# Optimization experiments

Hardware: AMD Instinct MI355X
Metric: run time of the kernel (lower is better)

## Reference

```python
import jax, jax.numpy as jnp
import numpy as np

HID = 2048      # hidden_size
NH = 16         # num_attention_heads
QLR = 1536      # q_lora_rank
KVLR = 512      # kv_lora_rank
DN = 128        # qk_nope_head_dim
DR = 64         # qk_rope_head_dim
DQK = DN + DR   # qk_head_dim = 192
DV = 128        # v_head_dim
EPS = 1e-6
THETA = 10000.0
B, T = 2, 2048


def rmsnorm(x, scale):
    return x * jax.lax.rsqrt(jnp.mean(x * x, axis=-1, keepdims=True) + EPS) * scale


def rope(x, positions):
    # x: [B, T, h, d]; NeoX-style rotate-half RoPE on the rope slice only
    d = x.shape[-1]
    inv_freq = 1.0 / (THETA ** (jnp.arange(0, d, 2, dtype=jnp.float32) / d))
    ang = positions.astype(jnp.float32)[..., None] * inv_freq       # [B, T, d/2]
    cos = jnp.cos(ang)[:, :, None, :]
    sin = jnp.sin(ang)[:, :, None, :]
    x1, x2 = jnp.split(x, 2, axis=-1)
    return jnp.concatenate([x1 * cos - x2 * sin, x2 * cos + x1 * sin], axis=-1).astype(x.dtype)


def setup_inputs() -> dict:
    key = jax.random.key(0)
    ks = jax.random.split(key, 8)
    s = 0.02
    x = jax.random.normal(ks[0], (B, T, HID), dtype=jnp.float32)
    attention_mask = jnp.ones((B, T), dtype=bool)
    positions = jnp.broadcast_to(jnp.arange(T, dtype=jnp.int32), (B, T))
    wqa = jax.random.normal(ks[1], (HID, QLR), dtype=jnp.float32) * s
    qa_scale = jnp.ones((QLR,), dtype=jnp.float32)
    wqb = jax.random.normal(ks[2], (QLR, NH * DQK), dtype=jnp.float32) * s
    wkva = jax.random.normal(ks[3], (HID, KVLR + DR), dtype=jnp.float32) * s
    kva_scale = jnp.ones((KVLR,), dtype=jnp.float32)
    wkvb = jax.random.normal(ks[4], (KVLR, NH * (DN + DV)), dtype=jnp.float32) * s
    wo = jax.random.normal(ks[5], (NH * DV, HID), dtype=jnp.float32) * s
    return {"x": x, "attention_mask": attention_mask, "positions": positions,
            "wqa": wqa, "qa_scale": qa_scale, "wqb": wqb,
            "wkva": wkva, "kva_scale": kva_scale, "wkvb": wkvb, "wo": wo}


def reference(x, attention_mask, positions, wqa, qa_scale, wqb, wkva, kva_scale, wkvb, wo):
    Bv, Tv, _ = x.shape
    # low-rank Q: hid -> q_lora_rank -> rmsnorm -> heads*qk_head_dim
    q = (rmsnorm(x @ wqa, qa_scale) @ wqb).reshape(Bv, Tv, NH, DQK)
    q_pass, q_rot = q[..., :DN], q[..., DN:]
    # compressed KV + shared rope key
    ckv = x @ wkva                                    # [B, T, KVLR + DR]
    kv_lat, k_rot = ckv[..., :KVLR], ckv[..., KVLR:].reshape(Bv, Tv, 1, DR)
    kv = (rmsnorm(kv_lat, kva_scale) @ wkvb).reshape(Bv, Tv, NH, DN + DV)
    k_pass, v = kv[..., :DN], kv[..., DN:]
    # decoupled RoPE on rope slice only
    q_rot = rope(q_rot, positions)
    k_rot = jnp.broadcast_to(rope(k_rot, positions), (Bv, Tv, NH, DR))
    q = jnp.concatenate([q_pass, q_rot], axis=-1)     # [B, T, H, 192]
    k = jnp.concatenate([k_pass, k_rot], axis=-1)
    # masked causal SDPA; v padding in the original is a no-op mathematically
    scale = DQK ** -0.5
    scores = jnp.einsum('bqhd,bkhd->bhqk', q, k) * scale
    causal = jnp.tril(jnp.ones((Tv, Tv), dtype=bool))
    mask = causal[None, None, :, :] & attention_mask[:, None, None, :].astype(bool)
    scores = jnp.where(mask, scores, jnp.finfo(scores.dtype).min)
    probs = jax.nn.softmax(scores, axis=-1)
    out = jnp.einsum('bhqk,bkhd->bqhd', probs, v).reshape(Bv, Tv, NH * DV)
    return out @ wo
```

## Files before the change

### kernel.cpp

```cpp
#include <hip/hip_runtime.h>
#include <math.h>
#include <stdint.h>

#define NHEAD 16
#define HIDDIM 2048
#define QLRANK 1536
#define KVRANK 512
#define DROT 64
#define BB 2
#define TT 2048
#define BTOK (BB*TT)
#define NPROJ 2304
#define CKV0 1536
#define ROT0 2048

typedef __bf16 bf16x8 __attribute__((ext_vector_type(8)));
typedef __bf16 bf16x4 __attribute__((ext_vector_type(4)));
typedef float f32x4 __attribute__((ext_vector_type(4)));
typedef uint16_t u16;
typedef uint32_t u32;

__device__ __forceinline__ u16 f2bf(float f) {
  union { float f; uint32_t u; } v; v.f = f;
  uint32_t r = v.u + 0x7fffu + ((v.u >> 16) & 1u);
  return (u16)(r >> 16);
}
__device__ __forceinline__ float bf2f(u16 h) {
  union { uint32_t u; float f; } v; v.u = ((uint32_t)h) << 16;
  return v.f;
}

__device__ __forceinline__ void gload_lds16(const u16* g, u16* l) {
  __builtin_amdgcn_global_load_lds(
      (const __attribute__((address_space(1))) uint32_t*)g,
      (__attribute__((address_space(3))) uint32_t*)l, 16, 0, 0);
}

__global__ __launch_bounds__(256) void cvt_f32_bf16(const float* __restrict__ in,
                                                    u16* __restrict__ out, int n) {
  int idx = (blockIdx.x * 256 + threadIdx.x) * 8;
  if (idx >= n) return;
  f32x4 a = *(const f32x4*)&in[idx];
  f32x4 b = *(const f32x4*)&in[idx + 4];
  union { f32x4 q; u16 e[8]; } w;
#pragma unroll
  for (int j = 0; j < 4; ++j) { w.e[j] = f2bf(a[j]); w.e[4 + j] = f2bf(b[j]); }
  *(f32x4*)&out[idx] = w.q;
}

__global__ __launch_bounds__(256) void transpose_w(const float* __restrict__ W,
                                                   u16* __restrict__ Wt,
                                                   int K, int N, int Npad, float scale,
                                                   const float* __restrict__ svec) {
  __shared__ float tile[32][33];
  int k0 = blockIdx.x * 32, n0 = blockIdx.y * 32;
  int tx = threadIdx.x, ty = threadIdx.y;
#pragma unroll
  for (int r = 0; r < 32; r += 8) {
    int k = k0 + ty + r, n = n0 + tx;
    tile[ty + r][tx] = (k < K && n < N) ? W[(size_t)k * N + n] : 0.f;
  }
  __syncthreads();
  float sv = scale * (svec ? svec[k0 + tx] : 1.f);
#pragma unroll
  for (int r = 0; r < 32; r += 8) {
    int n = n0 + ty + r, k = k0 + tx;
    if (n < Npad && k < K) Wt[(size_t)n * K + k] = f2bf(tile[tx][ty + r] * sv);
  }
}

template<int D>
__global__ __launch_bounds__(256) void row_invrms(const u16* __restrict__ in, int stride,
                                                  float* __restrict__ out) {
  const int row = blockIdx.x;
  const int tid = threadIdx.x;
  constexpr int NC = D / 8;
  float ss = 0.f;
  if (tid < NC) {
    union { f32x4 q; u16 e[8]; } t;
    t.q = *(const f32x4*)&in[(size_t)row * stride + tid * 8];
#pragma unroll
    for (int j = 0; j < 8; ++j) { float v = bf2f(t.e[j]); ss += v * v; }
  }
#pragma unroll
  for (int off = 1; off < 64; off <<= 1) ss += __shfl_xor(ss, off);
  __shared__ float red[4];
  if ((tid & 63) == 0) red[tid >> 6] = ss;
  __syncthreads();
  if (tid == 0)
    out[row] = rsqrtf((red[0] + red[1] + red[2] + red[3]) / (float)D + 1e-6f);
}

template<int OUTF32>
__global__ __launch_bounds__(256) void gemm_bt(const u16* __restrict__ A, int lda,
                                               const u16* __restrict__ Bt,
                                               void* __restrict__ Cv, int ldc,
                                               const float* __restrict__ rowscale,
                                               int N, int K) {
  __shared__ __align__(16) u16 As[2][128 * 32];
  __shared__ __align__(16) u16 Bs[2][128 * 32];
  const int tid = threadIdx.x;
  const int lane = tid & 63;
  const int wave = tid >> 6;
  const int bm = blockIdx.y * 128;
  const int bn = blockIdx.x * 128;
  const int wr = wave >> 1;
  const int wc = wave & 1;

  f32x4 acc[4][4] = {};

  const int srow = wave * 16 + (lane >> 2);
  const int scol = (lane & 3) * 8;
  const u16* Ag = A + (size_t)(bm + srow) * lda + scol;
  const u16* Bg = Bt + (size_t)(bn + srow) * K + scol;
  const int soff = (wave * 16) * 32;

  const int a_off = (wr * 64 + (lane & 15)) * 32 + (lane >> 4) * 8;
  const int b_off = (wc * 64 + (lane & 15)) * 32 + (lane >> 4) * 8;

  const int nt = K >> 5;

  gload_lds16(Ag, &As[0][soff]);
  gload_lds16(Ag + (size_t)64 * lda, &As[0][soff + 64 * 32]);
  gload_lds16(Bg, &Bs[0][soff]);
  gload_lds16(Bg + (size_t)64 * K, &Bs[0][soff + 64 * 32]);
  __syncthreads();

  int cur = 0;
  for (int t = 0; t < nt; ++t) {
    if (t + 1 < nt) {
      const int k0 = (t + 1) << 5;
      gload_lds16(Ag + k0, &As[cur ^ 1][soff]);
      gload_lds16(Ag + (size_t)64 * lda + k0, &As[cur ^ 1][soff + 64 * 32]);
      gload_lds16(Bg + k0, &Bs[cur ^ 1][soff]);
      gload_lds16(Bg + (size_t)64 * K + k0, &Bs[cur ^ 1][soff + 64 * 32]);
    }
    bf16x8 af[4], bfr[4];
#pragma unroll
    for (int m = 0; m < 4; ++m) af[m] = *(const bf16x8*)&As[cur][a_off + m * 16 * 32];
#pragma unroll
    for (int n = 0; n < 4; ++n) bfr[n] = *(const bf16x8*)&Bs[cur][b_off + n * 16 * 32];
#pragma unroll
    for (int m = 0; m < 4; ++m)
#pragma unroll
      for (int n = 0; n < 4; ++n)
        acc[m][n] = __builtin_amdgcn_mfma_f32_16x16x32_bf16(af[m], bfr[n], acc[m][n], 0, 0, 0);
    if (t + 1 < nt) {
      __syncthreads();
      cur ^= 1;
    }
  }

  const int row0 = bm + wr * 64 + (lane >> 4) * 4;
  const int col0 = bn + wc * 64 + (lane & 15);
#pragma unroll
  for (int m = 0; m < 4; ++m) {
    float rs[4] = {1.f, 1.f, 1.f, 1.f};
    if (rowscale) {
#pragma unroll
      for (int i = 0; i < 4; ++i) rs[i] = rowscale[row0 + m * 16 + i];
    }
#pragma unroll
    for (int n = 0; n < 4; ++n)
#pragma unroll
      for (int i = 0; i < 4; ++i) {
        size_t idx = (size_t)(row0 + m * 16 + i) * ldc + (col0 + n * 16);
        float v = acc[m][n][i] * rs[i];
        if (OUTF32) ((float*)Cv)[idx] = v;
        else        ((u16*)Cv)[idx] = f2bf(v);
      }
  }
}

template<int OUTF32>
__global__ __launch_bounds__(512, 2) void gemm256(const u16* __restrict__ A, int lda,
                                                  const u16* __restrict__ Bt,
                                                  void* __restrict__ Cv, int ldc,
                                                  const float* __restrict__ rowscale,
                                                  int K) {
  __shared__ __align__(16) u16 S[2][2][16384];
  const int tid = threadIdx.x, lane = tid & 63, wave = tid >> 6;
  const int l15 = lane & 15, l4 = lane >> 4;
  const int bm = blockIdx.y * 256, bn = blockIdx.x * 256;
  const int wm = wave >> 2, wn = wave & 3;

  const int rlo = lane >> 3;
  const int cbase = ((lane & 7) * 8) ^ ((lane >> 5) << 4);
  const u16* src[8];
  u16* dst[8];
#pragma unroll
  for (int j = 0; j < 8; ++j) {
    int gj = wave * 8 + j;
    if (gj < 32) {
      src[j] = A + (size_t)(bm + gj * 8 + rlo) * lda + cbase;
      dst[j] = &S[0][0][0] + gj * 512;
    } else {
      src[j] = Bt + (size_t)(bn + (gj - 32) * 8 + rlo) * K + cbase;
      dst[j] = &S[0][1][0] + (gj - 32) * 512;
    }
  }

  const int flip = ((l15 >> 2) & 1) << 5;
  const char* Sa0 = (const char*)&S[0][0][0] + wm * 16384;
  const char* Sb0 = (const char*)&S[0][1][0] + (wn >> 1) * 16384;
  const int arow0 = l15 * 128 + l4 * 16;
  const int brow0 = ((wn & 1) * 64 + l15) * 128 + l4 * 16;

  f32x4 acc[8][4] = {};
  const int nt = K >> 6;

#pragma unroll
  for (int j = 0; j < 8; ++j) gload_lds16(src[j], dst[j]);
#pragma unroll
  for (int j = 0; j < 8; ++j) gload_lds16(src[j] + 64, dst[j] + 32768);
  asm volatile("s_waitcnt vmcnt(8)" ::: "memory");
  __builtin_amdgcn_s_barrier();
  __builtin_amdgcn_sched_barrier(0);

  for (int t = 0; t < nt; ++t) {
    const char* Sab = Sa0 + (t & 1) * 65536;
    const char* Sbb = Sb0 + (t & 1) * 65536;
    bf16x8 bfr[4][2];
#pragma unroll
    for (int fn = 0; fn < 4; ++fn) {
      bfr[fn][0] = *(const bf16x8*)(Sbb + ((brow0 + fn * 2048) ^ flip));
      bfr[fn][1] = *(const bf16x8*)(Sbb + ((brow0 + fn * 2048 + 64) ^ flip));
    }
#pragma unroll
    for (int q = 0; q < 4; ++q) {
      bf16x8 a0[2], a1[2];
#pragma unroll
      for (int m2 = 0; m2 < 2; ++m2) {
        const int fm = q * 2 + m2;
        a0[m2] = *(const bf16x8*)(Sab + ((arow0 + fm * 2048) ^ flip));
        a1[m2] = *(const bf16x8*)(Sab + ((arow0 + fm * 2048 + 64) ^ flip));
      }
      __builtin_amdgcn_s_setprio(1);
#pragma unroll
      for (int m2 = 0; m2 < 2; ++m2)
#pragma unroll
        for (int fn = 0; fn < 4; ++fn) {
          f32x4 c = acc[q * 2 + m2][fn];
          c = __builtin_amdgcn_mfma_f32_16x16x32_bf16(a0[m2], bfr[fn][0], c, 0, 0, 0);
          c = __builtin_amdgcn_mfma_f32_16x16x32_bf16(a1[m2], bfr[fn][1], c, 0, 0, 0);
          acc[q * 2 + m2][fn] = c;
        }
      __builtin_amdgcn_s_setprio(0);
    }
    if (t + 1 < nt) {
      __builtin_amdgcn_s_barrier();
      __builtin_amdgcn_sched_barrier(0);
      if (t + 2 < nt) {
        const int koff = (t + 2) * 64;
#pragma unroll
        for (int j = 0; j < 8; ++j) gload_lds16(src[j] + koff, dst[j] + (t & 1) * 32768);
        asm volatile("s_waitcnt vmcnt(8)" ::: "memory");
      } else {
        asm volatile("s_waitcnt vmcnt(0)" ::: "memory");
      }
      __builtin_amdgcn_s_barrier();
      __builtin_amdgcn_sched_barrier(0);
    }
  }

  const int row0 = bm + wm * 128 + l4 * 4;
  const int col0 = bn + wn * 64 + l15;
#pragma unroll
  for (int fm = 0; fm < 8; ++fm) {
    float rs[4] = {1.f, 1.f, 1.f, 1.f};
    if (rowscale) {
#pragma unroll
      for (int i = 0; i < 4; ++i) rs[i] = rowscale[row0 + fm * 16 + i];
    }
#pragma unroll
    for (int fn = 0; fn < 4; ++fn)
#pragma unroll
      for (int i = 0; i < 4; ++i) {
        size_t idx = (size_t)(row0 + fm * 16 + i) * ldc + (col0 + fn * 16);
        float v = acc[fm][fn][i] * rs[i];
        if (OUTF32) ((float*)Cv)[idx] = v;
        else        ((u16*)Cv)[idx] = f2bf(v);
      }
  }
}

__global__ __launch_bounds__(256) void rope_table(const int* __restrict__ positions,
                                                  float2* __restrict__ tab) {
  int idx = blockIdx.x * 256 + threadIdx.x;
  if (idx >= BTOK * 32) return;
  int bt = idx >> 5, i = idx & 31;
  float invf = powf(10000.0f, -(float)i / 32.0f);
  float ang = (float)positions[bt] * invf;
  tab[idx] = make_float2(cosf(ang), sinf(ang));
}

__global__ __launch_bounds__(256) void rope_q(u16* __restrict__ q,
                                              const float2* __restrict__ tab) {
  int idx = blockIdx.x * 256 + threadIdx.x;
  if (idx >= BTOK * NHEAD * 32) return;
  int i = idx & 31;
  int h = (idx >> 5) & 15;
  int bt = idx >> 9;
  u16* p = q + (size_t)bt * 3072 + h * 192 + 128;
  float x1 = bf2f(p[i]), x2 = bf2f(p[32 + i]);
  float2 cs = tab[bt * 32 + i];
  p[i] = f2bf(x1 * cs.x - x2 * cs.y);
  p[32 + i] = f2bf(x2 * cs.x + x1 * cs.y);
}

__global__ __launch_bounds__(256) void assemble_k(const u16* __restrict__ kv,
                                                  const u16* __restrict__ proj,
                                                  const float2* __restrict__ tab,
                                                  u16* __restrict__ kf) {
  int bt = blockIdx.x;
  __shared__ __align__(16) u16 krot[64];
  int t = threadIdx.x;
  if (t < 64) {
    int i = t & 31;
    float2 cs = tab[bt * 32 + i];
    float x1 = bf2f(proj[(size_t)bt * NPROJ + ROT0 + i]);
    float x2 = bf2f(proj[(size_t)bt * NPROJ + ROT0 + 32 + i]);
    krot[t] = f2bf((t < 32) ? (x1 * cs.x - x2 * cs.y) : (x2 * cs.x + x1 * cs.y));
  }
  __syncthreads();
  for (int c = t; c < 16 * 24; c += 256) {
    int h = c / 24, seg = c % 24;
    u16* dst = kf + (size_t)bt * 3072 + h * 192 + seg * 8;
    if (seg < 16)
      *(f32x4*)dst = *(const f32x4*)&kv[(size_t)bt * 4096 + h * 256 + seg * 8];
    else
      *(f32x4*)dst = *(const f32x4*)&krot[(seg - 16) * 8];
  }
}

__device__ const int8_t JOB_QT[24] = {15,15,7,14,14,13,13,6,12,12,11,11,5,10,10,9,9,4,8,8,3,2,1,0};
__device__ const int8_t JOB_PC[24] = { 0, 1,2, 0, 1, 0, 1,2, 0, 1, 0, 1,2, 0, 1,0,1,2,0,1,2,2,2,2};

__global__ __launch_bounds__(256, 2) void attn_fwd5(const u16* __restrict__ Q,
                                                    const u16* __restrict__ Kf,
                                                    const u16* __restrict__ KV,
                                                    u16* __restrict__ O,
                                                    u16* __restrict__ Opart,
                                                    float2* __restrict__ ml) {
  __shared__ __align__(16) u16 Ks[2][64 * 192];
  __shared__ __align__(16) u16 Vs[2][64 * 128];

  const int tid = threadIdx.x, lane = tid & 63, wave = tid >> 6;
  const int l15 = lane & 15, l4 = lane >> 4;
  const int jobrank = blockIdx.x >> 5;
  const int bh = blockIdx.x & 31;
  const int qt = JOB_QT[jobrank];
  const int piece = JOB_PC[jobrank];
  const int q0 = qt * 128;
  const int b = bh >> 4, h = bh & 15;
  const int wq0 = q0 + wave * 32;

  bf16x8 qf[2][6];
#pragma unroll
  for (int m = 0; m < 2; ++m) {
    const u16* qp = Q + (size_t)(b * TT + wq0 + m * 16 + l15) * 3072 + h * 192 + l4 * 8;
#pragma unroll
    for (int kk = 0; kk < 6; ++kk) qf[m][kk] = *(const bf16x8*)(qp + kk * 32);
  }

  int ksrc[6];
#pragma unroll
  for (int j = 0; j < 6; ++j) {
    int o = (wave * 6 + j) * 1024 + lane * 16;
    int row = o / 384, col = o % 384;
    int scol = col ^ ((row & 7) << 4);
    ksrc[j] = row * 3072 + (scol >> 1);
  }
  int vsrc[4];
#pragma unroll
  for (int j = 0; j < 4; ++j) {
    int lam = (wave * 4 + j) * 512 + lane * 8;
    int kap = ((lam >> 6) & 15) * 4 + ((lam >> 4) & 3);
    int key = ((kap >> 5) & 1) * 32 + ((kap >> 2) & 3) * 8 + ((kap >> 4) & 1) * 4 + (kap & 3);
    int dv  = (lam >> 10) * 16 + (lam & 15);
    vsrc[j] = key * 4096 + dv;
  }
  const u16* Kbase = Kf + (size_t)(b * TT) * 3072 + h * 192;
  const u16* Vbase = KV + (size_t)(b * TT) * 4096 + h * 256 + 128;
  const int kofsW = wave * 3072;
  const int vofsW = wave * 2048;
  const unsigned vs_base = (unsigned)(uintptr_t)(&Vs[0][0]);

  f32x4 o_acc[2][8] = {};
  float m_r[2], l_r[2];
#pragma unroll
  for (int m = 0; m < 2; ++m) { m_r[m] = -INFINITY; l_r[m] = 0.f; }

  const int kt0 = (piece == 1) ? (qt + 1) : 0;
  const int kt1 = (piece == 0) ? (qt + 1) : (2 * qt + 2);

  {
    const u16* Kt = Kbase + (size_t)(kt0 * 64) * 3072;
    const u16* Vt = Vbase + (size_t)(kt0 * 64) * 4096;
#pragma unroll
    for (int j = 0; j < 6; ++j) gload_lds16(Kt + ksrc[j], &Ks[0][kofsW + j * 512]);
#pragma unroll
    for (int j = 0; j < 4; ++j) gload_lds16(Vt + vsrc[j], &Vs[0][vofsW + j * 512]);
  }

  for (int kt = kt0; kt < kt1; ++kt) {
    const int cur = (kt - kt0) & 1;
    __builtin_amdgcn_s_barrier();
    if (kt + 1 < kt1) {
      const u16* Kt = Kbase + (size_t)((kt + 1) * 64) * 3072;
      const u16* Vt = Vbase + (size_t)((kt + 1) * 64) * 4096;
#pragma unroll
      for (int j = 0; j < 6; ++j) gload_lds16(Kt + ksrc[j], &Ks[cur ^ 1][kofsW + j * 512]);
#pragma unroll
      for (int j = 0; j < 4; ++j) gload_lds16(Vt + vsrc[j], &Vs[cur ^ 1][vofsW + j * 512]);
      asm volatile("s_waitcnt vmcnt(10)" ::: "memory");
    } else {
      asm volatile("s_waitcnt vmcnt(0)" ::: "memory");
    }
    __builtin_amdgcn_s_barrier();
    __builtin_amdgcn_sched_barrier(0);

    if (kt * 64 > wq0 + 31) continue;
    const int kt64 = kt * 64;

    f32x4 s[2][4] = {};
    __builtin_amdgcn_s_setprio(1);
#pragma unroll
    for (int n = 0; n < 4; ++n) {
      const int krow = n * 16 + l15;
      const int swz = (l15 & 7) << 3;
#pragma unroll
      for (int kk = 0; kk < 6; ++kk) {
        bf16x8 kb = *(const bf16x8*)&Ks[cur][krow * 192 + ((kk * 32 + l4 * 8) ^ swz)];
        s[0][n] = __builtin_amdgcn_mfma_f32_16x16x32_bf16(kb, qf[0][kk], s[0][n], 0, 0, 0);
        s[1][n] = __builtin_amdgcn_mfma_f32_16x16x32_bf16(kb, qf[1][kk], s[1][n], 0, 0, 0);
      }
    }
    __builtin_amdgcn_s_setprio(0);

    u32 pk[2][4][2];
#pragma unroll
    for (int m = 0; m < 2; ++m) {
      const int qrow = wq0 + m * 16 + l15;
      const bool needmask = (kt64 + 63) > (wq0 + m * 16);
      if (needmask) {
#pragma unroll
        for (int n = 0; n < 4; ++n)
#pragma unroll
          for (int i = 0; i < 4; ++i)
            if (kt64 + n * 16 + l4 * 4 + i > qrow) s[m][n][i] = -INFINITY;
      }
      float pmax = -INFINITY;
#pragma unroll
      for (int n = 0; n < 4; ++n)
#pragma unroll
        for (int i = 0; i < 4; ++i) pmax = fmaxf(pmax, s[m][n][i]);
      pmax = fmaxf(pmax, __shfl_xor(pmax, 16));
      pmax = fmaxf(pmax, __shfl_xor(pmax, 32));

      if (!__all(pmax - m_r[m] <= 8.f)) {
        float mn = fmaxf(m_r[m], pmax);
        float alpha = __expf(m_r[m] - mn);
        m_r[m] = mn;
        l_r[m] *= alpha;
        float ab[4];
#pragma unroll
        for (int i = 0; i < 4; ++i) ab[i] = __shfl(alpha, l4 * 4 + i);
#pragma unroll
        for (int n = 0; n < 8; ++n)
#pragma unroll
          for (int i = 0; i < 4; ++i) o_acc[m][n][i] *= ab[i];
      }

      float psum = 0.f;
#pragma unroll
      for (int n = 0; n < 4; ++n) {
        float p0 = __expf(s[m][n][0] - m_r[m]);
        float p1 = __expf(s[m][n][1] - m_r[m]);
        float p2 = __expf(s[m][n][2] - m_r[m]);
        float p3 = __expf(s[m][n][3] - m_r[m]);
        psum += (p0 + p1) + (p2 + p3);
        union { u32 u; __bf16 e[2]; } a, c;
        a.e[0] = (__bf16)p0; a.e[1] = (__bf16)p1;
        c.e[0] = (__bf16)p2; c.e[1] = (__bf16)p3;
        pk[m][n][0] = a.u;
        pk[m][n][1] = c.u;
      }
      psum += __shfl_xor(psum, 16);
      psum += __shfl_xor(psum, 32);
      l_r[m] += psum;
    }

#pragma unroll
    for (int kk = 0; kk < 2; ++kk) {
      bf16x8 pa[2];
#pragma unroll
      for (int m = 0; m < 2; ++m) {
        union { u32 w[4]; bf16x8 v; } uu;
#pragma unroll
        for (int t = 0; t < 4; ++t) {
          int src = l15 + ((2 * (l4 & 1) + (t >> 1)) << 4);
          u32 a0 = __shfl(pk[m][2 * kk + 0][t & 1], src);
          u32 a1 = __shfl(pk[m][2 * kk + 1][t & 1], src);
          uu.w[t] = (l4 & 2) ? a1 : a0;
        }
        pa[m] = uu.v;
      }
      const unsigned va = vs_base + cur * 16384 + kk * 1024 + lane * 8;
#pragma unroll
      for (int g = 0; g < 2; ++g) {
        union { uint2 u; bf16x4 b; } lo[4], hi[4];
#pragma unroll
        for (int n = 0; n < 4; ++n) {
          unsigned a0 = va + (g * 4 + n) * 2048;
          asm volatile("ds_read_b64_tr_b16 %0, %1" : "=v"(lo[n].u) : "v"(a0));
          asm volatile("ds_read_b64_tr_b16 %0, %1 offset:512" : "=v"(hi[n].u) : "v"(a0));
        }
        asm volatile("s_waitcnt lgkmcnt(0)" ::: "memory");
        __builtin_amdgcn_sched_barrier(0);
        __builtin_amdgcn_s_setprio(1);
#pragma unroll
        for (int n = 0; n < 4; ++n) {
          bf16x8 vb = __builtin_shufflevector(lo[n].b, hi[n].b, 0, 1, 2, 3, 4, 5, 6, 7);
          o_acc[0][g * 4 + n] = __builtin_amdgcn_mfma_f32_16x16x32_bf16(pa[0], vb, o_acc[0][g * 4 + n], 0, 0, 0);
          o_acc[1][g * 4 + n] = __builtin_amdgcn_mfma_f32_16x16x32_bf16(pa[1], vb, o_acc[1][g * 4 + n], 0, 0, 0);
        }
        __builtin_amdgcn_s_setprio(0);
      }
    }
  }

  if (piece == 2) {
#pragma unroll
    for (int m = 0; m < 2; ++m) {
      float inv = 1.f / l_r[m];
      float li[4];
#pragma unroll
      for (int i = 0; i < 4; ++i) li[i] = __shfl(inv, l4 * 4 + i);
#pragma unroll
      for (int n = 0; n < 8; ++n)
#pragma unroll
        for (int i = 0; i < 4; ++i) {
          int r = wq0 + m * 16 + l4 * 4 + i;
          O[(size_t)(b * TT + r) * 2048 + h * 128 + n * 16 + l15] = f2bf(o_acc[m][n][i] * li[i]);
        }
    }
  } else {
    const size_t pidx = ((size_t)(qt - 8) * 32 + bh) * 2 + piece;
    u16* op = Opart + pidx * (128 * 128);
    float2* mlp = ml + pidx * 128;
#pragma unroll
    for (int m = 0; m < 2; ++m)
#pragma unroll
      for (int n = 0; n < 8; ++n)
#pragma unroll
        for (int i = 0; i < 4; ++i)
          op[(wave * 32 + m * 16 + l4 * 4 + i) * 128 + n * 16 + l15] = f2bf(o_acc[m][n][i]);
    if (l4 == 0) {
#pragma unroll
      for (int m = 0; m < 2; ++m)
        mlp[wave * 32 + m * 16 + l15] = make_float2(m_r[m], l_r[m]);
    }
  }
}

__global__ __launch_bounds__(256) void attn_combine(const u16* __restrict__ Opart,
                                                    const float2* __restrict__ ml,
                                                    u16* __restrict__ O) {
  int gid = blockIdx.x * 256 + threadIdx.x;
  int dvseg = gid & 15;
  int row = (gid >> 4) & 127;
  int bh = (gid >> 11) & 31;
  int qt8 = gid >> 16;
  size_t i1 = ((size_t)qt8 * 32 + bh) * 2;
  float2 ml1 = ml[i1 * 128 + row], ml2 = ml[(i1 + 1) * 128 + row];
  float m = fmaxf(ml1.x, ml2.x);
  float w1 = __expf(ml1.x - m), w2 = __expf(ml2.x - m);
  float inv = 1.f / (w1 * ml1.y + w2 * ml2.y);
  union { f32x4 q; u16 e[8]; } a, bq, w;
  a.q  = *(const f32x4*)&Opart[i1 * 16384 + row * 128 + dvseg * 8];
  bq.q = *(const f32x4*)&Opart[(i1 + 1) * 16384 + row * 128 + dvseg * 8];
#pragma unroll
  for (int j = 0; j < 8; ++j)
    w.e[j] = f2bf((w1 * bf2f(a.e[j]) + w2 * bf2f(bq.e[j])) * inv);
  int b = bh >> 4, h = bh & 15;
  int r = 1024 + qt8 * 128 + row;
  *(f32x4*)&O[(size_t)(b * TT + r) * 2048 + h * 128 + dvseg * 8] = w.q;
}

extern "C" void kernel_launch(void* const* d_in, const int* in_sizes, int n_in,
                              void* d_out, int out_size, void* d_ws, size_t ws_size,
                              hipStream_t stream) {
  (void)in_sizes; (void)n_in; (void)out_size; (void)ws_size;
  const float* x         = (const float*)d_in[0];
  const int*   positions = (const int*)d_in[2];
  const float* wqa       = (const float*)d_in[3];
  const float* qa_scale  = (const float*)d_in[4];
  const float* wqb       = (const float*)d_in[5];
  const float* wkva      = (const float*)d_in[6];
  const float* kva_scale = (const float*)d_in[7];
  const float* wkvb      = (const float*)d_in[8];
  const float* wo        = (const float*)d_in[9];
  float* out = (float*)d_out;

  char* wsp = (char*)d_ws;
  auto alloc = [&](size_t bytes) {
    char* p = wsp; wsp += (bytes + 255) & ~(size_t)255; return p;
  };
  u16* xb      = (u16*)alloc((size_t)BTOK * HIDDIM * 2);
  u16* proj_t  = (u16*)alloc((size_t)NPROJ * HIDDIM * 2);
  u16* wqb_t   = (u16*)alloc((size_t)3072 * QLRANK * 2);
  u16* wkvb_t  = (u16*)alloc((size_t)4096 * KVRANK * 2);
  u16* wo_t    = (u16*)alloc((size_t)HIDDIM * HIDDIM * 2);
  u16* proj    = (u16*)alloc((size_t)BTOK * NPROJ * 2);
  u16* q       = (u16*)alloc((size_t)BTOK * 3072 * 2);
  u16* kv      = (u16*)alloc((size_t)BTOK * 4096 * 2);
  u16* kf      = (u16*)alloc((size_t)BTOK * 3072 * 2);
  float2* tab  = (float2*)alloc((size_t)BTOK * 32 * 8);
  float* invq  = (float*)alloc((size_t)BTOK * 4);
  float* invkv = (float*)alloc((size_t)BTOK * 4);
  float2* mlbuf= (float2*)alloc((size_t)8 * 32 * 2 * 128 * 8);
  u16* ao = xb;
  u16* Opart = proj;

  dim3 blk(256);
  dim3 blk512(512);
  const float qscale = 0.07216878364870322f;

  cvt_f32_bf16<<<(BTOK * HIDDIM / 8 + 255) / 256, blk, 0, stream>>>(x, xb, BTOK * HIDDIM);
  {
    dim3 tb(32, 8);
    transpose_w<<<dim3(HIDDIM / 32, QLRANK / 32), tb, 0, stream>>>(wqa, proj_t, HIDDIM, QLRANK, QLRANK, 1.f, nullptr);
    transpose_w<<<dim3(HIDDIM / 32, (NPROJ - CKV0) / 32), tb, 0, stream>>>(wkva, proj_t + (size_t)CKV0 * HIDDIM, HIDDIM, 576, NPROJ - CKV0, 1.f, nullptr);
    transpose_w<<<dim3(QLRANK / 32, 3072 / 32), tb, 0, stream>>>(wqb, wqb_t, QLRANK, 3072, 3072, qscale, qa_scale);
    transpose_w<<<dim3(KVRANK / 32, 4096 / 32), tb, 0, stream>>>(wkvb, wkvb_t, KVRANK, 4096, 4096, 1.f, kva_scale);
    transpose_w<<<dim3(HIDDIM / 32, HIDDIM / 32), tb, 0, stream>>>(wo, wo_t, HIDDIM, HIDDIM, HIDDIM, 1.f, nullptr);
  }
  rope_table<<<(BTOK * 32 + 255) / 256, blk, 0, stream>>>(positions, tab);

  gemm_bt<0><<<dim3(NPROJ / 128, BTOK / 128), blk, 0, stream>>>(xb, HIDDIM, proj_t, proj, NPROJ, nullptr, NPROJ, HIDDIM);

  row_invrms<QLRANK><<<BTOK, blk, 0, stream>>>(proj, NPROJ, invq);
  row_invrms<KVRANK><<<BTOK, blk, 0, stream>>>(proj + CKV0, NPROJ, invkv);

  gemm256<0><<<dim3(3072 / 256, BTOK / 256), blk512, 0, stream>>>(proj, NPROJ, wqb_t, q, 3072, invq, QLRANK);
  gemm256<0><<<dim3(4096 / 256, BTOK / 256), blk512, 0, stream>>>(proj + CKV0, NPROJ, wkvb_t, kv, 4096, invkv, KVRANK);

  rope_q<<<(BTOK * NHEAD * 32 + 255) / 256, blk, 0, stream>>>(q, tab);
  assemble_k<<<BTOK, blk, 0, stream>>>(kv, proj, tab, kf);

  attn_fwd5<<<dim3(24 * 32), blk, 0, stream>>>(q, kf, kv, ao, Opart, mlbuf);
  attn_combine<<<(8 * 32 * 128 * 16) / 256, blk, 0, stream>>>(Opart, mlbuf, ao);

  gemm_bt<1><<<dim3(HIDDIM / 128, BTOK / 128), blk, 0, stream>>>(ao, HIDDIM, wo_t, out, HIDDIM, nullptr, HIDDIM, HIDDIM);
}
```

Measured before the change: 350.4 us.

## Rework LDS swizzle in gemm256 and simplify attention to single-buffered LDS with P staging

In gemm256 the XOR swizzle changes from a 2-bit flip to a full 8-way row-based XOR on 16-byte column chunks, to reduce LDS bank conflicts on fragment reads. The attention kernel drops K/V double buffering: each tile is now loaded synchronously between two __syncthreads. The P matrix is written to a per-wave padded LDS buffer and read back as MFMA A-fragments, replacing the cross-lane shuffle transpose. This halves K/V LDS use and removes shuffle work, but gives up overlap of global loads with compute.

```diff
diff --git a/kernel.cpp b/kernel.cpp
--- a/kernel.cpp
+++ b/kernel.cpp
@@ -185,7 +185,7 @@
   const int wm = wave >> 2, wn = wave & 3;
 
   const int rlo = lane >> 3;
-  const int cbase = ((lane & 7) * 8) ^ ((lane >> 5) << 4);
+  const int cbase = (((lane & 7) ^ (rlo & 7)) * 8);
   const u16* src[8];
   u16* dst[8];
 #pragma unroll
@@ -200,11 +200,12 @@
     }
   }
 
-  const int flip = ((l15 >> 2) & 1) << 5;
+  const int r7 = l15 & 7;
+  const int acol = (l4 ^ r7) * 16;
   const char* Sa0 = (const char*)&S[0][0][0] + wm * 16384;
   const char* Sb0 = (const char*)&S[0][1][0] + (wn >> 1) * 16384;
-  const int arow0 = l15 * 128 + l4 * 16;
-  const int brow0 = ((wn & 1) * 64 + l15) * 128 + l4 * 16;
+  const int arow0 = l15 * 128;
+  const int brow0 = ((wn & 1) * 64 + l15) * 128;
 
   f32x4 acc[8][4] = {};
   const int nt = K >> 6;
@@ -223,8 +224,8 @@
     bf16x8 bfr[4][2];
 #pragma unroll
     for (int fn = 0; fn < 4; ++fn) {
-      bfr[fn][0] = *(const bf16x8*)(Sbb + ((brow0 + fn * 2048) ^ flip));
-      bfr[fn][1] = *(const bf16x8*)(Sbb + ((brow0 + fn * 2048 + 64) ^ flip));
+      bfr[fn][0] = *(const bf16x8*)(Sbb + brow0 + fn * 2048 + acol);
+      bfr[fn][1] = *(const bf16x8*)(Sbb + brow0 + fn * 2048 + (acol ^ 64));
     }
 #pragma unroll
     for (int q = 0; q < 4; ++q) {
@@ -232,8 +233,8 @@
 #pragma unroll
       for (int m2 = 0; m2 < 2; ++m2) {
         const int fm = q * 2 + m2;
-        a0[m2] = *(const bf16x8*)(Sab + ((arow0 + fm * 2048) ^ flip));
-        a1[m2] = *(const bf16x8*)(Sab + ((arow0 + fm * 2048 + 64) ^ flip));
+        a0[m2] = *(const bf16x8*)(Sab + arow0 + fm * 2048 + acol);
+        a1[m2] = *(const bf16x8*)(Sab + arow0 + fm * 2048 + (acol ^ 64));
       }
       __builtin_amdgcn_s_setprio(1);
 #pragma unroll
@@ -336,14 +337,15 @@
 __device__ const int8_t JOB_QT[24] = {15,15,7,14,14,13,13,6,12,12,11,11,5,10,10,9,9,4,8,8,3,2,1,0};
 __device__ const int8_t JOB_PC[24] = { 0, 1,2, 0, 1, 0, 1,2, 0, 1, 0, 1,2, 0, 1,0,1,2,0,1,2,2,2,2};
 
-__global__ __launch_bounds__(256, 2) void attn_fwd5(const u16* __restrict__ Q,
+__global__ __launch_bounds__(256, 2) void attn_fwd6(const u16* __restrict__ Q,
                                                     const u16* __restrict__ Kf,
                                                     const u16* __restrict__ KV,
                                                     u16* __restrict__ O,
                                                     u16* __restrict__ Opart,
                                                     float2* __restrict__ ml) {
-  __shared__ __align__(16) u16 Ks[2][64 * 192];
-  __shared__ __align__(16) u16 Vs[2][64 * 128];
+  __shared__ __align__(16) u16 Ks[64 * 192];
+  __shared__ __align__(16) u16 Vs[64 * 128];
+  __shared__ __align__(16) u16 Ps[4][32][72];
 
   const int tid = threadIdx.x, lane = tid & 63, wave = tid >> 6;
   const int l15 = lane & 15, l4 = lane >> 4;
@@ -382,9 +384,9 @@
   }
   const u16* Kbase = Kf + (size_t)(b * TT) * 3072 + h * 192;
   const u16* Vbase = KV + (size_t)(b * TT) * 4096 + h * 256 + 128;
-  const int kofsW = wave * 3072;
-  const int vofsW = wave * 2048;
-  const unsigned vs_base = (unsigned)(uintptr_t)(&Vs[0][0]);
+  u16* KsW = Ks + (wave * 6) * 512;
+  u16* VsW = Vs + (wave * 4) * 512;
+  const unsigned vs_base = (unsigned)(uintptr_t)(&Vs[0]);
 
   f32x4 o_acc[2][8] = {};
   float m_r[2], l_r[2];
@@ -394,31 +396,15 @@
   const int kt0 = (piece == 1) ? (qt + 1) : 0;
   const int kt1 = (piece == 0) ? (qt + 1) : (2 * qt + 2);
 
-  {
-    const u16* Kt = Kbase + (size_t)(kt0 * 64) * 3072;
-    const u16* Vt = Vbase + (size_t)(kt0 * 64) * 4096;
-#pragma unroll
-    for (int j = 0; j < 6; ++j) gload_lds16(Kt + ksrc[j], &Ks[0][kofsW + j * 512]);
-#pragma unroll
-    for (int j = 0; j < 4; ++j) gload_lds16(Vt + vsrc[j], &Vs[0][vofsW + j * 512]);
-  }
-
   for (int kt = kt0; kt < kt1; ++kt) {
-    const int cur = (kt - kt0) & 1;
-    __builtin_amdgcn_s_barrier();
-    if (kt + 1 < kt1) {
-      const u16* Kt = Kbase + (size_t)((kt + 1) * 64) * 3072;
-      const u16* Vt = Vbase + (size_t)((kt + 1) * 64) * 4096;
-#pragma unroll
-      for (int j = 0; j < 6; ++j) gload_lds16(Kt + ksrc[j], &Ks[cur ^ 1][kofsW + j * 512]);
-#pragma unroll
-      for (int j = 0; j < 4; ++j) gload_lds16(Vt + vsrc[j], &Vs[cur ^ 1][vofsW + j * 512]);
-      asm volatile("s_waitcnt vmcnt(10)" ::: "memory");
-    } else {
-      asm volatile("s_waitcnt vmcnt(0)" ::: "memory");
-    }
-    __builtin_amdgcn_s_barrier();
-    __builtin_amdgcn_sched_barrier(0);
+    __syncthreads();
+    const u16* Kt = Kbase + (size_t)(kt * 64) * 3072;
+    const u16* Vt = Vbase + (size_t)(kt * 64) * 4096;
+#pragma unroll
+    for (int j = 0; j < 6; ++j) gload_lds16(Kt + ksrc[j], KsW + j * 512);
+#pragma unroll
+    for (int j = 0; j < 4; ++j) gload_lds16(Vt + vsrc[j], VsW + j * 512);
+    __syncthreads();
 
     if (kt * 64 > wq0 + 31) continue;
     const int kt64 = kt * 64;
@@ -431,14 +417,13 @@
       const int swz = (l15 & 7) << 3;
 #pragma unroll
       for (int kk = 0; kk < 6; ++kk) {
-        bf16x8 kb = *(const bf16x8*)&Ks[cur][krow * 192 + ((kk * 32 + l4 * 8) ^ swz)];
+        bf16x8 kb = *(const bf16x8*)&Ks[krow * 192 + ((kk * 32 + l4 * 8) ^ swz)];
         s[0][n] = __builtin_amdgcn_mfma_f32_16x16x32_bf16(kb, qf[0][kk], s[0][n], 0, 0, 0);
         s[1][n] = __builtin_amdgcn_mfma_f32_16x16x32_bf16(kb, qf[1][kk], s[1][n], 0, 0, 0);
       }
     }
     __builtin_amdgcn_s_setprio(0);
 
-    u32 pk[2][4][2];
 #pragma unroll
     for (int m = 0; m < 2; ++m) {
       const int qrow = wq0 + m * 16 + l15;
@@ -480,33 +465,25 @@
         float p2 = __expf(s[m][n][2] - m_r[m]);
         float p3 = __expf(s[m][n][3] - m_r[m]);
         psum += (p0 + p1) + (p2 + p3);
-        union { u32 u; __bf16 e[2]; } a, c;
-        a.e[0] = (__bf16)p0; a.e[1] = (__bf16)p1;
-        c.e[0] = (__bf16)p2; c.e[1] = (__bf16)p3;
-        pk[m][n][0] = a.u;
-        pk[m][n][1] = c.u;
+        union { uint2 d; u16 e[4]; } pw;
+        pw.e[0] = f2bf(p0); pw.e[1] = f2bf(p1);
+        pw.e[2] = f2bf(p2); pw.e[3] = f2bf(p3);
+        *(uint2*)&Ps[wave][m * 16 + l15][n * 16 + l4 * 4] = pw.d;
       }
       psum += __shfl_xor(psum, 16);
       psum += __shfl_xor(psum, 32);
       l_r[m] += psum;
     }
 
+    asm volatile("s_waitcnt lgkmcnt(0)" ::: "memory");
+    __builtin_amdgcn_sched_barrier(0);
+
 #pragma unroll
     for (int kk = 0; kk < 2; ++kk) {
       bf16x8 pa[2];
-#pragma unroll
-      for (int m = 0; m < 2; ++m) {
-        union { u32 w[4]; bf16x8 v; } uu;
-#pragma unroll
-        for (int t = 0; t < 4; ++t) {
-          int src = l15 + ((2 * (l4 & 1) + (t >> 1)) << 4);
-          u32 a0 = __shfl(pk[m][2 * kk + 0][t & 1], src);
-          u32 a1 = __shfl(pk[m][2 * kk + 1][t & 1], src);
-          uu.w[t] = (l4 & 2) ? a1 : a0;
-        }
-        pa[m] = uu.v;
-      }
-      const unsigned va = vs_base + cur * 16384 + kk * 1024 + lane * 8;
+      pa[0] = *(const bf16x8*)&Ps[wave][l15][kk * 32 + l4 * 8];
+      pa[1] = *(const bf16x8*)&Ps[wave][16 + l15][kk * 32 + l4 * 8];
+      const unsigned va = vs_base + kk * 1024 + lane * 8;
 #pragma unroll
       for (int g = 0; g < 2; ++g) {
         union { uint2 u; bf16x4 b; } lo[4], hi[4];
@@ -649,7 +626,7 @@
   rope_q<<<(BTOK * NHEAD * 32 + 255) / 256, blk, 0, stream>>>(q, tab);
   assemble_k<<<BTOK, blk, 0, stream>>>(kv, proj, tab, kf);
 
-  attn_fwd5<<<dim3(24 * 32), blk, 0, stream>>>(q, kf, kv, ao, Opart, mlbuf);
+  attn_fwd6<<<dim3(24 * 32), blk, 0, stream>>>(q, kf, kv, ao, Opart, mlbuf);
   attn_combine<<<(8 * 32 * 128 * 16) / 256, blk, 0, stream>>>(Opart, mlbuf, ao);
 
   gemm_bt<1><<<dim3(HIDDIM / 128, BTOK / 128), blk, 0, stream>>>(ao, HIDDIM, wo_t, out, HIDDIM, nullptr, HIDDIM, HIDDIM);
```

New measurement: 333.6 us. -4.8%, faster.
